# Kernel tuning notes

Measured on AMD Instinct MI355X. Metric: run time of the kernel, lower is better.

Reference implementation:

```python
import jax, jax.numpy as jnp
import numpy as np

NUM_CLASS = 4096
HIDDEN = 512
N_GROUPS = 64  # per branch (co and cl)
BATCH = 64


def _make_group_of(rng, n_groups, num_class):
    # Ragged partition of [0, num_class) into n_groups contiguous segments,
    # mirroring len_co_list_index offsets of the original module.
    cuts = np.sort(rng.choice(np.arange(1, num_class), size=n_groups - 1, replace=False))
    sizes = np.diff(np.concatenate([[0], cuts, [num_class]]))
    return np.repeat(np.arange(n_groups), sizes)  # [num_class] -> group id per class slot


def setup_inputs() -> dict:
    key = jax.random.key(0)
    k_x, k_cow, k_clw, k_cob, k_clb = jax.random.split(key, 5)
    rng = np.random.default_rng(0)
    stdv = 1.0 / np.sqrt(HIDDEN)  # matches reset_parameters uniform(-stdv, stdv)

    x = jax.random.normal(k_x, (BATCH, 2 * N_GROUPS, HIDDEN), dtype=jnp.float32)
    co_W = jax.random.uniform(k_cow, (1, NUM_CLASS, HIDDEN), jnp.float32, -stdv, stdv)
    cl_W = jax.random.uniform(k_clw, (1, NUM_CLASS, HIDDEN), jnp.float32, -stdv, stdv)
    co_b = jax.random.uniform(k_cob, (1, NUM_CLASS), jnp.float32, -stdv, stdv)
    cl_b = jax.random.uniform(k_clb, (1, NUM_CLASS), jnp.float32, -stdv, stdv)

    co_group_of = jnp.asarray(_make_group_of(rng, N_GROUPS, NUM_CLASS), jnp.int32)
    cl_group_of = jnp.asarray(_make_group_of(rng, N_GROUPS, NUM_CLASS), jnp.int32)
    # co_index / cl_index are class-id permutations applied after concat
    co_index = jnp.asarray(rng.permutation(NUM_CLASS), jnp.int32)
    cl_index = jnp.asarray(rng.permutation(NUM_CLASS), jnp.int32)

    return {
        "x": x,
        "co_W": co_W, "cl_W": cl_W,
        "co_b": co_b, "cl_b": cl_b,
        "co_group_of": co_group_of, "cl_group_of": cl_group_of,
        "co_index": co_index, "cl_index": cl_index,
        "group_len": N_GROUPS,
    }


def reference(x, co_W, cl_W, co_b, cl_b, co_group_of, cl_group_of, co_index, cl_index, group_len):
    # x: [B, 2*G, H]; first G group-features feed the co branch, rest the cl branch.
    co_x = x[:, :group_len, :]   # [B, G, H]
    cl_x = x[:, group_len:, :]   # [B, G, H]

    # Fused ragged group-wise broadcast-multiply + reduce:
    # out[b, c] = dot(W[0, c], x[b, group_of[c]]) + b[0, c]
    co_out = jnp.einsum("bch,ch->bc", co_x[:, co_group_of, :], co_W[0]) + co_b  # [B, C]
    cl_out = jnp.einsum("bch,ch->bc", cl_x[:, cl_group_of, :], cl_W[0]) + cl_b  # [B, C]

    # Final index_select gather over classes
    return co_out[:, co_index], cl_out[:, cl_index]
```

## Files before the change

### kernel.cpp

```cpp
#include <hip/hip_runtime.h>
#include <hip/hip_bf16.h>
#include <string.h>

#define NUM_CLASS 4096
#define HIDDEN    512
#define NGROUPS   64
#define BATCH     64

#define WS_NWORK 0
#define WS_WORK  16
#define WS_SRC   2048
#define WS_INV   10240
#define TMP_OFF_F 32768
#define TMP_H_STRIDE (128*4096)
#define TMP_S_STRIDE (2*128*4096)

typedef __attribute__((ext_vector_type(8))) short short8;
typedef __attribute__((ext_vector_type(4))) float f32x4;

__device__ __forceinline__ unsigned int pack2bf(float a, float b) {
    __hip_bfloat16 ha = __float2bfloat16(a), hb = __float2bfloat16(b);
    unsigned short ua, ub;
    memcpy(&ua, &ha, 2); memcpy(&ub, &hb, 2);
    return (unsigned int)ua | ((unsigned int)ub << 16);
}

template<bool WITH_INV>
__global__ __launch_bounds__(1024) void prep_kernel(
    const int* __restrict__ co_gof, const int* __restrict__ cl_gof,
    const int* __restrict__ co_idx, const int* __restrict__ cl_idx,
    int* __restrict__ ws)
{
    __shared__ int s_starts[2][65];
    __shared__ int s_wbase[2][64];
    int tid = threadIdx.x;
    for (int v = tid; v < 2 * NUM_CLASS; v += 1024) {
        int h = v >> 12, c = v & (NUM_CLASS - 1);
        const int* gof = h ? cl_gof : co_gof;
        int g = gof[c];
        if (c == 0) { s_starts[h][0] = 0; s_starts[h][64] = NUM_CLASS; }
        else if (g != gof[c - 1]) s_starts[h][g] = c;
    }
    __syncthreads();
    if (tid < 64) {
        int lane = tid;
        for (int h = 0; h < 2; ++h) {
            int s = s_starts[h][lane], e = s_starts[h][lane + 1];
            int cnt = (e - s + 63) >> 6;
            int inc = cnt;
            #pragma unroll
            for (int d = 1; d < 64; d <<= 1) {
                int o = __shfl_up(inc, d, 64);
                if (lane >= d) inc += o;
            }
            int excl = inc - cnt;
            s_wbase[h][lane] = excl;
            for (int t = 0; t < cnt; ++t) {
                int c0 = s + t * 64;
                int ncls = min(64, e - c0);
                ws[WS_WORK + h * 128 + excl + t] = (lane << 20) | (ncls << 12) | c0;
            }
            if (lane == 63) ws[WS_NWORK + h] = inc;
        }
    }
    __syncthreads();
    for (int v = tid; v < 2 * NUM_CLASS; v += 1024) {
        int h = v >> 12, c = v & (NUM_CLASS - 1);
        const int* gof = h ? cl_gof : co_gof;
        int g = gof[c];
        int rel = c - s_starts[h][g];
        ws[WS_SRC + v] = (s_wbase[h][g] + (rel >> 6)) * 64 + (rel & 63);
        if (WITH_INV) {
            const int* idx = h ? cl_idx : co_idx;
            ws[WS_INV + h * NUM_CLASS + idx[c]] = c;
        }
    }
}

template<int KS, bool SCATTER>
__global__ __launch_bounds__(256, 2) void gwl_stage1(
    const float* __restrict__ x,
    const float* __restrict__ co_W, const float* __restrict__ cl_W,
    const float* __restrict__ co_b, const float* __restrict__ cl_b,
    int* __restrict__ ws, float* __restrict__ out)
{
    const int nblk = 128 * 2 * KS;
    const int chunk = nblk >> 3;
    int bid = blockIdx.x;
    int swz = (bid & 7) * chunk + (bid >> 3);
    int widx = swz & 127;
    int hk   = swz >> 7;
    int h    = hk & 1;
    int kh   = hk >> 1;

    int nw = ws[WS_NWORK + h];
    if (widx >= nw) return;
    int packed = ws[WS_WORK + h * 128 + widx];
    int c0 = packed & 0xFFF, ncls = (packed >> 12) & 0xFF, g = packed >> 20;
    const float* Wp = h ? cl_W : co_W;
    int xrow = h * 64 + g;

    __shared__ __align__(16) unsigned char smem[2][18432];

    int tid = threadIdx.x;
    int l = tid & 63, w = tid >> 6;

    int rowq[4], kvq[4], wcl[4];
    #pragma unroll
    for (int q = 0; q < 4; ++q) {
        int v = q * 256 + tid;
        rowq[q] = v >> 4;
        kvq[q]  = v & 15;
        wcl[q]  = min(rowq[q], ncls - 1);
    }

    float4 rxA[4], rwA[4], rxB[4], rwB[4];
    f32x4 acc[4];
    #pragma unroll
    for (int i = 0; i < 4; ++i) acc[i] = (f32x4)(0.0f);

    const int NCH = 8 / KS;
    const int kbase = kh * (HIDDEN / KS);

#define LOADC(T, RX, RW) do {                                                       \
    int k0_ = kbase + (T) * 64;                                                     \
    _Pragma("unroll")                                                               \
    for (int q = 0; q < 4; ++q) {                                                   \
        RX[q] = *(const float4*)(x + rowq[q] * 65536 + xrow * 512 + k0_ + kvq[q]*4);\
        RW[q] = *(const float4*)(Wp + (c0 + wcl[q]) * 512 + k0_ + kvq[q] * 4);      \
    } } while (0)

#define STOREC(BUF, RX, RW) do {                                                    \
    unsigned short (*Xs_)[72]  = (unsigned short(*)[72])smem[BUF];                  \
    unsigned short (*Wls_)[72] = (unsigned short(*)[72])(smem[BUF] + 9216);         \
    _Pragma("unroll")                                                               \
    for (int q = 0; q < 4; ++q) {                                                   \
        unsigned int x0 = pack2bf(RX[q].x, RX[q].y);                                \
        unsigned int x1 = pack2bf(RX[q].z, RX[q].w);                                \
        unsigned int w0 = pack2bf(RW[q].x, RW[q].y);                                \
        unsigned int w1 = pack2bf(RW[q].z, RW[q].w);                                \
        *(uint2*)&Xs_[rowq[q]][kvq[q] * 4]  = make_uint2(x0, x1);                   \
        *(uint2*)&Wls_[rowq[q]][kvq[q] * 4] = make_uint2(w0, w1);                   \
    } } while (0)

#define COMPUTEC(BUF) do {                                                          \
    unsigned short (*Xs_)[72]  = (unsigned short(*)[72])smem[BUF];                  \
    unsigned short (*Wls_)[72] = (unsigned short(*)[72])(smem[BUF] + 9216);         \
    _Pragma("unroll")                                                               \
    for (int kq = 0; kq < 2; ++kq) {                                                \
        int koff = kq * 32 + (l >> 4) * 8;                                          \
        short8 bfrag = *(const short8*)&Wls_[w * 16 + (l & 15)][koff];              \
        _Pragma("unroll")                                                           \
        for (int i = 0; i < 4; ++i) {                                               \
            short8 afrag = *(const short8*)&Xs_[16 * i + (l & 15)][koff];           \
            acc[i] = __builtin_amdgcn_mfma_f32_16x16x32_bf16(afrag, bfrag, acc[i],  \
                                                             0, 0, 0);              \
        }                                                                           \
    } } while (0)

    LOADC(0, rxA, rwA);
    LOADC(1, rxB, rwB);
    STOREC(0, rxA, rwA);
    __syncthreads();
    #pragma unroll
    for (int t = 0; t < NCH; ++t) {
        if (t + 2 < NCH) {
            if (t & 1) LOADC(t + 2, rxB, rwB);
            else       LOADC(t + 2, rxA, rwA);
        }
        if (t + 1 < NCH) {
            if (t & 1) STOREC((t + 1) & 1, rxA, rwA);
            else       STOREC((t + 1) & 1, rxB, rwB);
        }
        COMPUTEC(t & 1);
        __syncthreads();
    }

    float (*ftile)[65] = (float(*)[65])smem[0];
    #pragma unroll
    for (int i = 0; i < 4; ++i)
        #pragma unroll
        for (int r = 0; r < 4; ++r)
            ftile[w * 16 + (l & 15)][16 * i + (l >> 4) * 4 + r] = acc[i][r];
    __syncthreads();

    if (!SCATTER) {
        float* tile = (float*)ws + TMP_OFF_F
                    + (size_t)(kh * 2 + h) * TMP_H_STRIDE + (size_t)widx * 4096;
        #pragma unroll
        for (int p = 0; p < 4; ++p) {
            int f = p * 256 + tid;
            int slot = f >> 4, b4 = (f & 15) * 4;
            *(float4*)&tile[slot * 64 + b4] = *(const float4*)&ftile[slot][b4];
        }
    } else {
        const float* bias = h ? cl_b : co_b;
        const int*   inv  = ws + WS_INV + h * NUM_CLASS;
        float* outh = out + (size_t)h * BATCH * NUM_CLASS;
        #pragma unroll
        for (int p = 0; p < 4; ++p) {
            int f = p * 256 + tid;
            int slot = f >> 4, b4 = (f & 15) * 4;
            if (slot < ncls) {
                int c = c0 + slot;
                int oc = inv[c];
                float bb = bias[c];
                #pragma unroll
                for (int e = 0; e < 4; ++e)
                    outh[(b4 + e) * 4096 + oc] = ftile[slot][b4 + e] + bb;
            }
        }
    }
#undef LOADC
#undef STOREC
#undef COMPUTEC
}

template<int KS>
__global__ __launch_bounds__(256) void gwl_permute(
    const int* __restrict__ ws,
    const float* __restrict__ co_b, const float* __restrict__ cl_b,
    const int* __restrict__ co_idx, const int* __restrict__ cl_idx,
    float* __restrict__ out)
{
    int jc = blockIdx.x;
    int h  = blockIdx.y;
    const float* bias   = h ? cl_b : co_b;
    const int*   idx    = h ? cl_idx : co_idx;
    const int*   srcoff = ws + WS_SRC + h * NUM_CLASS;
    const float* tmph   = (const float*)ws + TMP_OFF_F + (size_t)h * TMP_H_STRIDE;

    __shared__ float tile[64][65];
    int tid = threadIdx.x;
    int lane = tid & 63, w = tid >> 6;

    #pragma unroll
    for (int u = 0; u < 16; ++u) {
        int jj = u * 4 + w;
        int j  = jc * 64 + jj;
        int c  = idx[j];
        int rc = srcoff[c];
        float v = bias[c];
        #pragma unroll
        for (int s = 0; s < KS; ++s)
            v += tmph[(size_t)s * TMP_S_STRIDE + (size_t)rc * 64 + lane];
        tile[lane][jj] = v;
    }
    __syncthreads();

    #pragma unroll
    for (int p = 0; p < 4; ++p) {
        int f = p * 256 + tid;
        int b = f >> 4, j4 = (f & 15) * 4;
        *(float4*)&out[((size_t)h * 64 + b) * 4096 + jc * 64 + j4] =
            *(const float4*)&tile[b][j4];
    }
}

extern "C" void kernel_launch(void* const* d_in, const int* in_sizes, int n_in,
                              void* d_out, int out_size, void* d_ws, size_t ws_size,
                              hipStream_t stream)
{
    (void)in_sizes; (void)n_in; (void)out_size;
    const float* x      = (const float*)d_in[0];
    const float* co_W   = (const float*)d_in[1];
    const float* cl_W   = (const float*)d_in[2];
    const float* co_b   = (const float*)d_in[3];
    const float* cl_b   = (const float*)d_in[4];
    const int*   co_gof = (const int*)d_in[5];
    const int*   cl_gof = (const int*)d_in[6];
    const int*   co_idx = (const int*)d_in[7];
    const int*   cl_idx = (const int*)d_in[8];
    int*   ws  = (int*)d_ws;
    float* out = (float*)d_out;

    const size_t base  = (size_t)TMP_OFF_F * 4;
    const size_t slice = (size_t)TMP_S_STRIDE * 4;

    if (ws_size >= base + 2 * slice) {
        hipLaunchKernelGGL((prep_kernel<false>), dim3(1), dim3(1024), 0, stream,
                           co_gof, cl_gof, co_idx, cl_idx, ws);
        hipLaunchKernelGGL((gwl_stage1<2, false>), dim3(512), dim3(256), 0, stream,
                           x, co_W, cl_W, co_b, cl_b, ws, out);
        hipLaunchKernelGGL((gwl_permute<2>), dim3(64, 2), dim3(256), 0, stream,
                           ws, co_b, cl_b, co_idx, cl_idx, out);
    } else if (ws_size >= base + 1 * slice) {
        hipLaunchKernelGGL((prep_kernel<false>), dim3(1), dim3(1024), 0, stream,
                           co_gof, cl_gof, co_idx, cl_idx, ws);
        hipLaunchKernelGGL((gwl_stage1<1, false>), dim3(256), dim3(256), 0, stream,
                           x, co_W, cl_W, co_b, cl_b, ws, out);
        hipLaunchKernelGGL((gwl_permute<1>), dim3(64, 2), dim3(256), 0, stream,
                           ws, co_b, cl_b, co_idx, cl_idx, out);
    } else {
        hipLaunchKernelGGL((prep_kernel<true>), dim3(1), dim3(1024), 0, stream,
                           co_gof, cl_gof, co_idx, cl_idx, ws);
        hipLaunchKernelGGL((gwl_stage1<1, true>), dim3(256), dim3(256), 0, stream,
                           x, co_W, cl_W, co_b, cl_b, ws, out);
    }
}
```

Baseline: 23.79 us.

## Index partial sums by class id, drop src map, add 4-way K split

```diff
diff --git a/kernel.cpp b/kernel.cpp
--- a/kernel.cpp
+++ b/kernel.cpp
@@ -9,11 +9,10 @@
 
 #define WS_NWORK 0
 #define WS_WORK  16
-#define WS_SRC   2048
 #define WS_INV   10240
-#define TMP_OFF_F 32768
-#define TMP_H_STRIDE (128*4096)
-#define TMP_S_STRIDE (2*128*4096)
+#define TMP_OFF_F 16384
+#define TMP_H_STRIDE (4096*64)
+#define TMP_S_STRIDE (2*4096*64)
 
 typedef __attribute__((ext_vector_type(8))) short short8;
 typedef __attribute__((ext_vector_type(4))) float f32x4;
@@ -32,7 +31,6 @@
     int* __restrict__ ws)
 {
     __shared__ int s_starts[2][65];
-    __shared__ int s_wbase[2][64];
     int tid = threadIdx.x;
     for (int v = tid; v < 2 * NUM_CLASS; v += 1024) {
         int h = v >> 12, c = v & (NUM_CLASS - 1);
@@ -40,6 +38,10 @@
         int g = gof[c];
         if (c == 0) { s_starts[h][0] = 0; s_starts[h][64] = NUM_CLASS; }
         else if (g != gof[c - 1]) s_starts[h][g] = c;
+        if (WITH_INV) {
+            const int* idx = h ? cl_idx : co_idx;
+            ws[WS_INV + h * NUM_CLASS + idx[c]] = c;
+        }
     }
     __syncthreads();
     if (tid < 64) {
@@ -54,7 +56,6 @@
                 if (lane >= d) inc += o;
             }
             int excl = inc - cnt;
-            s_wbase[h][lane] = excl;
             for (int t = 0; t < cnt; ++t) {
                 int c0 = s + t * 64;
                 int ncls = min(64, e - c0);
@@ -63,22 +64,10 @@
             if (lane == 63) ws[WS_NWORK + h] = inc;
         }
     }
-    __syncthreads();
-    for (int v = tid; v < 2 * NUM_CLASS; v += 1024) {
-        int h = v >> 12, c = v & (NUM_CLASS - 1);
-        const int* gof = h ? cl_gof : co_gof;
-        int g = gof[c];
-        int rel = c - s_starts[h][g];
-        ws[WS_SRC + v] = (s_wbase[h][g] + (rel >> 6)) * 64 + (rel & 63);
-        if (WITH_INV) {
-            const int* idx = h ? cl_idx : co_idx;
-            ws[WS_INV + h * NUM_CLASS + idx[c]] = c;
-        }
-    }
 }
 
 template<int KS, bool SCATTER>
-__global__ __launch_bounds__(256, 2) void gwl_stage1(
+__global__ __launch_bounds__(256, 4) void gwl_stage1(
     const float* __restrict__ x,
     const float* __restrict__ co_W, const float* __restrict__ cl_W,
     const float* __restrict__ co_b, const float* __restrict__ cl_b,
@@ -159,7 +148,7 @@
     } } while (0)
 
     LOADC(0, rxA, rwA);
-    LOADC(1, rxB, rwB);
+    if (NCH > 1) LOADC(1, rxB, rwB);
     STOREC(0, rxA, rwA);
     __syncthreads();
     #pragma unroll
@@ -185,13 +174,14 @@
     __syncthreads();
 
     if (!SCATTER) {
-        float* tile = (float*)ws + TMP_OFF_F
-                    + (size_t)(kh * 2 + h) * TMP_H_STRIDE + (size_t)widx * 4096;
+        float* tmph = (float*)ws + TMP_OFF_F + (size_t)(kh * 2 + h) * TMP_H_STRIDE;
         #pragma unroll
         for (int p = 0; p < 4; ++p) {
             int f = p * 256 + tid;
             int slot = f >> 4, b4 = (f & 15) * 4;
-            *(float4*)&tile[slot * 64 + b4] = *(const float4*)&ftile[slot][b4];
+            if (slot < ncls)
+                *(float4*)&tmph[(size_t)(c0 + slot) * 64 + b4] =
+                    *(const float4*)&ftile[slot][b4];
         }
     } else {
         const float* bias = h ? cl_b : co_b;
@@ -225,10 +215,9 @@
 {
     int jc = blockIdx.x;
     int h  = blockIdx.y;
-    const float* bias   = h ? cl_b : co_b;
-    const int*   idx    = h ? cl_idx : co_idx;
-    const int*   srcoff = ws + WS_SRC + h * NUM_CLASS;
-    const float* tmph   = (const float*)ws + TMP_OFF_F + (size_t)h * TMP_H_STRIDE;
+    const float* bias = h ? cl_b : co_b;
+    const int*   idx  = h ? cl_idx : co_idx;
+    const float* tmph = (const float*)ws + TMP_OFF_F + (size_t)h * TMP_H_STRIDE;
 
     __shared__ float tile[64][65];
     int tid = threadIdx.x;
@@ -239,11 +228,10 @@
         int jj = u * 4 + w;
         int j  = jc * 64 + jj;
         int c  = idx[j];
-        int rc = srcoff[c];
         float v = bias[c];
         #pragma unroll
         for (int s = 0; s < KS; ++s)
-            v += tmph[(size_t)s * TMP_S_STRIDE + (size_t)rc * 64 + lane];
+            v += tmph[(size_t)s * TMP_S_STRIDE + (size_t)c * 64 + lane];
         tile[lane][jj] = v;
     }
     __syncthreads();
@@ -277,7 +265,14 @@
     const size_t base  = (size_t)TMP_OFF_F * 4;
     const size_t slice = (size_t)TMP_S_STRIDE * 4;
 
-    if (ws_size >= base + 2 * slice) {
+    if (ws_size >= base + 4 * slice) {
+        hipLaunchKernelGGL((prep_kernel<false>), dim3(1), dim3(1024), 0, stream,
+                           co_gof, cl_gof, co_idx, cl_idx, ws);
+        hipLaunchKernelGGL((gwl_stage1<4, false>), dim3(1024), dim3(256), 0, stream,
+                           x, co_W, cl_W, co_b, cl_b, ws, out);
+        hipLaunchKernelGGL((gwl_permute<4>), dim3(64, 2), dim3(256), 0, stream,
+                           ws, co_b, cl_b, co_idx, cl_idx, out);
+    } else if (ws_size >= base + 2 * slice) {
         hipLaunchKernelGGL((prep_kernel<false>), dim3(1), dim3(1024), 0, stream,
                            co_gof, cl_gof, co_idx, cl_idx, ws);
         hipLaunchKernelGGL((gwl_stage1<2, false>), dim3(512), dim3(256), 0, stream,
```

Measured after the change: 22.97 us. -3.5%, faster.
